# Performance work log

Hardware: AMD Instinct MI355X
Metric: run time of the kernel (lower is better)

The kernel has to match this reference:

```python
import jax, jax.numpy as jnp
import numpy as np

DIM = 768
NUM_HEADS = 12
HEAD_DIM = DIM // NUM_HEADS
BASE = 10000.0


def rotate_half(x):
    x1, x2 = jnp.split(x, 2, axis=-1)
    return jnp.concatenate((-x2, x1), axis=-1)


def rope_cos_sin(seq_len, dim, dtype):
    inv_freq = 1.0 / (BASE ** (jnp.arange(0, dim, 2, dtype=jnp.float32) / dim))
    t = jnp.arange(seq_len, dtype=jnp.float32)
    freqs = jnp.einsum('i,j->ij', t, inv_freq)  # [N, dim/2]
    emb = jnp.concatenate((freqs, freqs), axis=-1)  # [N, dim]
    return jnp.cos(emb).astype(dtype), jnp.sin(emb).astype(dtype)


def setup_inputs() -> dict:
    key = jax.random.key(0)
    k1, k2, k3, k4 = jax.random.split(key, 4)
    B, N, C = 1, 4096, DIM
    x = jax.random.normal(k1, (B, N, C), dtype=jnp.float32)
    s = 1.0 / np.sqrt(C)
    qkv_w = jax.random.normal(k2, (3 * C, C), dtype=jnp.float32) * s
    proj_w = jax.random.normal(k3, (C, C), dtype=jnp.float32) * s
    proj_b = jax.random.normal(k4, (C,), dtype=jnp.float32) * 0.01
    return {"x": x, "qkv_w": qkv_w, "proj_w": proj_w, "proj_b": proj_b}


def reference(x, qkv_w, proj_w, proj_b):
    B, N, C = x.shape
    H, D = NUM_HEADS, HEAD_DIM
    scale = D ** -0.5
    qkv = jnp.einsum('bnc,oc->bno', x, qkv_w)           # [B, N, 3C]
    qkv = qkv.reshape(B, N, 3, H, D).transpose(2, 0, 3, 1, 4)  # [3, B, H, N, D]
    q, k, v = qkv[0], qkv[1], qkv[2]
    cos, sin = rope_cos_sin(N, D, x.dtype)              # [N, D] each
    cos = cos[None, None]                               # [1,1,N,D]
    sin = sin[None, None]
    q = q * cos + rotate_half(q) * sin
    k = k * cos + rotate_half(k) * sin
    attn = jnp.einsum('bhqd,bhkd->bhqk', q, k) * scale  # [B,H,N,N]
    attn = jax.nn.softmax(attn, axis=-1)
    out = jnp.einsum('bhqk,bhkd->bhqd', attn, v)        # [B,H,N,D]
    out = out.transpose(0, 2, 1, 3).reshape(B, N, C)
    return jnp.einsum('bnc,oc->bno', out, proj_w) + proj_b
```

## Files before the change

### kernel.cpp

```cpp
#include <hip/hip_runtime.h>
#include <hip/hip_bf16.h>
#include <math.h>

#define DIM 768
#define NHEADS 12
#define HD 64
#define SEQ 4096
#define KSPLIT 4

typedef __bf16 bf16x8 __attribute__((ext_vector_type(8)));
typedef float f32x4 __attribute__((ext_vector_type(4)));

__device__ inline ushort f2bf(float f) {
    __bf16 b = (__bf16)f;
    union { __bf16 b; ushort u; } v; v.b = b;
    return v.u;
}

__device__ inline ushort f2bf_tw(float f) {
    union { float f; uint u; } v; v.f = f;
    uint r = v.u + 0x7FFF + ((v.u >> 16) & 1);
    return (ushort)(r >> 16);
}

__global__ __launch_bounds__(256)
void cvt_bf16(const float* __restrict__ src, ushort* __restrict__ dst, int n4)
{
    const int i = blockIdx.x * 256 + threadIdx.x;
    if (i >= n4) return;
    const float4 v = ((const float4*)src)[i];
    ushort4 w;
    w.x = f2bf(v.x); w.y = f2bf(v.y); w.z = f2bf(v.z); w.w = f2bf(v.w);
    ((ushort4*)dst)[i] = w;
}

__global__ __launch_bounds__(256)
void rope_tab_k(float2* __restrict__ tab)
{
    const int idx = blockIdx.x * 256 + threadIdx.x;
    const int j = idx & 31;
    const int n = idx >> 5;
    const float invf = (float)pow(10000.0, -(double)j / 32.0);
    const float ang  = (float)n * invf;
    double s, c;
    sincos((double)ang, &s, &c);
    tab[idx] = make_float2((float)c, (float)s);
}

__global__ __launch_bounds__(256)
void gemm_qkv(const ushort* __restrict__ A, const ushort* __restrict__ B,
              const float2* __restrict__ tab,
              ushort* __restrict__ Qb, ushort* __restrict__ Kb,
              ushort* __restrict__ Vp)
{
    constexpr int BM = 128, BN = 128, BK = 64, PAD = 8;
    __shared__ ushort Ah[BM][BK + PAD];
    __shared__ ushort Bh[BN][BK + PAD];

    const int t    = threadIdx.x;
    const int lane = t & 63;
    const int wv   = t >> 6;
    const int wm   = (wv >> 1) * 64;
    const int wn   = (wv & 1) * 64;
    const int m0   = blockIdx.y * BM;
    const int n0   = blockIdx.x * BN;

    f32x4 acc[4][4] = {};

    const int srow = t >> 3;
    const int sseg = (t & 7) * 8;

    for (int k0 = 0; k0 < DIM; k0 += BK) {
        #pragma unroll
        for (int i = 0; i < 4; ++i) {
            const int row = srow + i * 32;
            *(float4*)&Ah[row][sseg] =
                *(const float4*)&A[(size_t)(m0 + row) * DIM + k0 + sseg];
            *(float4*)&Bh[row][sseg] =
                *(const float4*)&B[(size_t)(n0 + row) * DIM + k0 + sseg];
        }
        __syncthreads();

        #pragma unroll
        for (int ks = 0; ks < BK; ks += 32) {
            const int koff = ks + ((lane >> 4) << 3);
            const int rs = lane & 15;
            bf16x8 af[4], bf[4];
            #pragma unroll
            for (int i = 0; i < 4; ++i) {
                af[i] = *(const bf16x8*)&Ah[wm + i * 16 + rs][koff];
                bf[i] = *(const bf16x8*)&Bh[wn + i * 16 + rs][koff];
            }
            #pragma unroll
            for (int i = 0; i < 4; ++i)
                #pragma unroll
                for (int j = 0; j < 4; ++j)
                    acc[i][j] = __builtin_amdgcn_mfma_f32_16x16x32_bf16(
                        af[i], bf[j], acc[i][j], 0, 0, 0);
        }
        __syncthreads();
    }

    const int rsel  = lane & 15;
    const int quad  = lane >> 4;
    const int rbase = m0 + wm + (quad << 2);
    const int c0    = n0 + wn;
    const int tt    = c0 / DIM;
    const int h     = (c0 % DIM) >> 6;

    if (tt == 2) {
        const int T = (m0 + wm) >> 6;
        #pragma unroll
        for (int j = 0; j < 4; ++j) {
            const int d = rsel + 16 * j;
            ushort vv[16];
            #pragma unroll
            for (int r = 0; r < 4; ++r)
                #pragma unroll
                for (int i = 0; i < 4; ++i)
                    vv[4 * r + i] = f2bf(acc[i][j][r]);
            ushort* dst = &Vp[((size_t)h * HD + d) * SEQ + T * 64 + 16 * quad];
            *(float4*)&dst[0] = *(const float4*)&vv[0];
            *(float4*)&dst[8] = *(const float4*)&vv[8];
        }
    } else {
        ushort* dstb = (tt == 0 ? Qb : Kb) + (size_t)h * SEQ * HD;
        const float qs = (tt == 0) ? 0.18033688011112042f : 1.0f;
        #pragma unroll
        for (int i = 0; i < 4; ++i)
            #pragma unroll
            for (int r = 0; r < 4; ++r) {
                const int n = rbase + i * 16 + r;
                #pragma unroll
                for (int j = 0; j < 2; ++j) {
                    const float a = acc[i][j][r];
                    const float b = acc[i][j + 2][r];
                    const float2 cs2 = tab[n * 32 + rsel + 16 * j];
                    dstb[(size_t)n * HD + rsel + 16 * j]      = f2bf((a * cs2.x - b * cs2.y) * qs);
                    dstb[(size_t)n * HD + rsel + 16 * j + 32] = f2bf((b * cs2.x + a * cs2.y) * qs);
                }
            }
    }
}

__global__ __launch_bounds__(256, 4)
void flash_mfma(const ushort* __restrict__ Qb, const ushort* __restrict__ Kb,
                const ushort* __restrict__ Vp,
                float* __restrict__ Opart, float* __restrict__ lpart)
{
    __shared__ ushort Ks[64][68];
    __shared__ ushort Vs[64][68];
    __shared__ ushort Pl[4][32][68];

    const int t    = threadIdx.x;
    const int lane = t & 63;
    const int wv   = t >> 6;
    const int rsel = lane & 15;
    const int quad = lane >> 4;

    const int p  = blockIdx.x + 32 * (blockIdx.y + 12 * blockIdx.z);
    const int c  = p & 7;
    const int r  = p >> 3;
    const int gi = r >> 5;
    const int xq = r & 31;
    const int g  = gi * 8 + c;
    const int h    = g % 12;
    const int part = g / 12;

    const int q0   = xq * 128 + wv * 32;
    const int Tbeg = (part * (SEQ / KSPLIT)) >> 6;
    const int Tend = Tbeg + (SEQ / KSPLIT) / 64;

    const int crow = t >> 2;
    const int ccol = (t & 3) * 16;

    bf16x8 aq[2][2];
    #pragma unroll
    for (int mi = 0; mi < 2; ++mi)
        #pragma unroll
        for (int ks = 0; ks < 2; ++ks)
            aq[mi][ks] = *(const bf16x8*)&Qb[((size_t)h * SEQ + q0 + 16 * mi + rsel) * HD
                                             + ks * 32 + quad * 8];

    f32x4 accO[2][4] = {};
    float lsum[2][4] = {};

    for (int T = Tbeg; T < Tend; ++T) {
        __syncthreads();
        {
            const ushort* ksrc = &Kb[((size_t)h * SEQ + T * 64 + crow) * HD + ccol];
            *(float4*)&Ks[crow][ccol]     = *(const float4*)&ksrc[0];
            *(float4*)&Ks[crow][ccol + 8] = *(const float4*)&ksrc[8];
            const ushort* vsrc = &Vp[((size_t)h * HD + crow) * SEQ + T * 64 + ccol];
            *(float4*)&Vs[crow][ccol]     = *(const float4*)&vsrc[0];
            *(float4*)&Vs[crow][ccol + 8] = *(const float4*)&vsrc[8];
        }
        __syncthreads();

        bf16x8 bk[4][2], bv[4][2];
        #pragma unroll
        for (int n = 0; n < 4; ++n)
            #pragma unroll
            for (int ks = 0; ks < 2; ++ks) {
                bk[n][ks] = *(const bf16x8*)&Ks[16 * n + rsel][32 * ks + quad * 8];
                bv[n][ks] = *(const bf16x8*)&Vs[16 * n + rsel][32 * ks + quad * 8];
            }

        #pragma unroll
        for (int mi = 0; mi < 2; ++mi) {
            f32x4 accS[4] = {};
            #pragma unroll
            for (int ks = 0; ks < 2; ++ks)
                #pragma unroll
                for (int n = 0; n < 4; ++n)
                    accS[n] = __builtin_amdgcn_mfma_f32_16x16x32_bf16(
                        aq[mi][ks], bk[n][ks], accS[n], 0, 0, 0);

            #pragma unroll
            for (int r = 0; r < 4; ++r) {
                const float p0 = __builtin_amdgcn_exp2f(accS[0][r]);
                const float p1 = __builtin_amdgcn_exp2f(accS[1][r]);
                const float p2 = __builtin_amdgcn_exp2f(accS[2][r]);
                const float p3 = __builtin_amdgcn_exp2f(accS[3][r]);
                ushort4 pw;
                pw.x = f2bf_tw(p0); pw.y = f2bf_tw(p1);
                pw.z = f2bf_tw(p2); pw.w = f2bf_tw(p3);
                *(ushort4*)&Pl[wv][16 * mi + 4 * quad + r][4 * rsel] = pw;
                lsum[mi][r] += (p0 + p1) + (p2 + p3);
            }
        }

        asm volatile("s_waitcnt lgkmcnt(0)" ::: "memory");

        #pragma unroll
        for (int mi = 0; mi < 2; ++mi) {
            bf16x8 ap[2];
            ap[0] = *(const bf16x8*)&Pl[wv][16 * mi + rsel][quad * 8];
            ap[1] = *(const bf16x8*)&Pl[wv][16 * mi + rsel][32 + quad * 8];
            #pragma unroll
            for (int ks = 0; ks < 2; ++ks)
                #pragma unroll
                for (int j = 0; j < 4; ++j)
                    accO[mi][j] = __builtin_amdgcn_mfma_f32_16x16x32_bf16(
                        ap[ks], bv[j][ks], accO[mi][j], 0, 0, 0);
        }
    }

    #pragma unroll
    for (int mi = 0; mi < 2; ++mi)
        #pragma unroll
        for (int r = 0; r < 4; ++r) {
            float s = lsum[mi][r];
            s += __shfl_xor(s, 1);
            s += __shfl_xor(s, 2);
            s += __shfl_xor(s, 4);
            s += __shfl_xor(s, 8);
            lsum[mi][r] = s;
        }

    float* Ob = Opart + ((size_t)part * NHEADS + h) * SEQ * HD;
    float* lb = lpart + ((size_t)part * NHEADS + h) * SEQ;
    #pragma unroll
    for (int mi = 0; mi < 2; ++mi)
        #pragma unroll
        for (int r = 0; r < 4; ++r) {
            const int n = q0 + 16 * mi + 4 * quad + r;
            #pragma unroll
            for (int j = 0; j < 4; ++j)
                Ob[(size_t)n * HD + 16 * j + rsel] = accO[mi][j][r];
            if (rsel == 0) lb[n] = lsum[mi][r];
        }
}

__global__ __launch_bounds__(256)
void merge_k(const float* __restrict__ Opart, const float* __restrict__ lpart,
             ushort* __restrict__ AO)
{
    const int idx = blockIdx.x * 256 + threadIdx.x;
    const int dg = idx & 15;
    const int n  = (idx >> 4) & (SEQ - 1);
    const int h  = idx >> 16;

    float4 o = make_float4(0.f, 0.f, 0.f, 0.f);
    float l = 0.f;
    #pragma unroll
    for (int p = 0; p < KSPLIT; ++p) {
        const float4 v = *(const float4*)&Opart[(((size_t)p * NHEADS + h) * SEQ + n) * HD + dg * 4];
        o.x += v.x; o.y += v.y; o.z += v.z; o.w += v.w;
        l += lpart[((size_t)p * NHEADS + h) * SEQ + n];
    }
    const float inv = 1.f / l;
    ushort4 w;
    w.x = f2bf(o.x * inv); w.y = f2bf(o.y * inv);
    w.z = f2bf(o.z * inv); w.w = f2bf(o.w * inv);
    *(ushort4*)&AO[(size_t)n * DIM + h * HD + dg * 4] = w;
}

__global__ __launch_bounds__(256)
void gemm_proj(const ushort* __restrict__ A, const ushort* __restrict__ B,
               const float* __restrict__ bias, float* __restrict__ out)
{
    constexpr int BM = 128, BN = 128, BK = 64, PAD = 8;
    __shared__ ushort As[BM][BK + PAD];
    __shared__ ushort Bs[BN][BK + PAD];

    const int t    = threadIdx.x;
    const int lane = t & 63;
    const int wv   = t >> 6;
    const int wm   = (wv >> 1) * 64;
    const int wn   = (wv & 1) * 64;
    const int m0   = blockIdx.y * BM;
    const int n0   = blockIdx.x * BN;

    f32x4 acc[4][4] = {};

    const int srow = t >> 3;
    const int sseg = (t & 7) * 8;

    for (int k0 = 0; k0 < DIM; k0 += BK) {
        #pragma unroll
        for (int i = 0; i < 4; ++i) {
            const int row = srow + i * 32;
            *(float4*)&As[row][sseg] =
                *(const float4*)&A[(size_t)(m0 + row) * DIM + k0 + sseg];
            *(float4*)&Bs[row][sseg] =
                *(const float4*)&B[(size_t)(n0 + row) * DIM + k0 + sseg];
        }
        __syncthreads();

        #pragma unroll
        for (int ks = 0; ks < BK; ks += 32) {
            const int koff = ks + ((lane >> 4) << 3);
            const int rs = lane & 15;
            bf16x8 af[4], bf[4];
            #pragma unroll
            for (int i = 0; i < 4; ++i) {
                af[i] = *(const bf16x8*)&As[wm + i * 16 + rs][koff];
                bf[i] = *(const bf16x8*)&Bs[wn + i * 16 + rs][koff];
            }
            #pragma unroll
            for (int i = 0; i < 4; ++i)
                #pragma unroll
                for (int j = 0; j < 4; ++j)
                    acc[i][j] = __builtin_amdgcn_mfma_f32_16x16x32_bf16(
                        af[i], bf[j], acc[i][j], 0, 0, 0);
        }
        __syncthreads();
    }

    const int rbase = m0 + wm + ((lane >> 4) << 2);
    const int cbase = n0 + wn + (lane & 15);

    #pragma unroll
    for (int j = 0; j < 4; ++j) {
        const int col = cbase + j * 16;
        const float bv = bias[col];
        #pragma unroll
        for (int i = 0; i < 4; ++i) {
            const int row0 = rbase + i * 16;
            #pragma unroll
            for (int r = 0; r < 4; ++r)
                out[(size_t)(row0 + r) * DIM + col] = acc[i][j][r] + bv;
        }
    }
}

extern "C" void kernel_launch(void* const* d_in, const int* in_sizes, int n_in,
                              void* d_out, int out_size, void* d_ws, size_t ws_size,
                              hipStream_t stream)
{
    const float* x      = (const float*)d_in[0];
    const float* qkv_w  = (const float*)d_in[1];
    const float* proj_w = (const float*)d_in[2];
    const float* proj_b = (const float*)d_in[3];

    const size_t headsz = (size_t)NHEADS * SEQ * HD;
    char* p = (char*)d_ws;
    ushort* Qb    = (ushort*)p;                 p += headsz * 2;
    ushort* Kb    = (ushort*)p;                 p += headsz * 2;
    ushort* Vp    = (ushort*)p;                 p += headsz * 2;
    ushort* AO    = (ushort*)p;                 p += (size_t)SEQ * DIM * 2;
    float*  Opart = (float*)p;                  p += (size_t)KSPLIT * headsz * 4;
    float*  lpart = (float*)p;                  p += (size_t)KSPLIT * NHEADS * SEQ * 4;
    float2* tab   = (float2*)p;                 p += (size_t)SEQ * 32 * sizeof(float2);
    ushort* xb    = (ushort*)p;                 p += (size_t)SEQ * DIM * 2;
    ushort* qwb   = (ushort*)p;                 p += (size_t)3 * DIM * DIM * 2;
    ushort* pwb   = (ushort*)p;
    float*  out   = (float*)d_out;

    rope_tab_k<<<(SEQ * 32) / 256, 256, 0, stream>>>(tab);
    cvt_bf16<<<(SEQ * DIM / 4) / 256, 256, 0, stream>>>(x, xb, SEQ * DIM / 4);
    cvt_bf16<<<(3 * DIM * DIM / 4) / 256, 256, 0, stream>>>(qkv_w, qwb, 3 * DIM * DIM / 4);
    cvt_bf16<<<(DIM * DIM / 4) / 256, 256, 0, stream>>>(proj_w, pwb, DIM * DIM / 4);

    gemm_qkv<<<dim3(3 * DIM / 128, SEQ / 128), 256, 0, stream>>>(
        xb, qwb, tab, Qb, Kb, Vp);

    flash_mfma<<<dim3(SEQ / 128, NHEADS, KSPLIT), 256, 0, stream>>>(
        Qb, Kb, Vp, Opart, lpart);

    merge_k<<<(NHEADS * SEQ * 16) / 256, 256, 0, stream>>>(Opart, lpart, AO);

    gemm_proj<<<dim3(DIM / 128, SEQ / 128), 256, 0, stream>>>(
        AO, pwb, proj_b, out);
}
```

Baseline: 223.0 us.

## Double-buffer K/V tiles in flash attention with register prefetch

Adds a second LDS buffer for the K and V tiles. The next tile's global loads are issued into registers at the top of each iteration and written to the alternate buffer after the compute, leaving one barrier per iteration instead of two. The goal is to hide global load latency behind the MFMA and softmax work. In exchange it uses more LDS and registers, and the launch-bounds occupancy hint drops from 4 to 3 blocks per CU.

```diff
diff --git a/kernel.cpp b/kernel.cpp
--- a/kernel.cpp
+++ b/kernel.cpp
@@ -143,13 +143,13 @@
     }
 }
 
-__global__ __launch_bounds__(256, 4)
+__global__ __launch_bounds__(256, 3)
 void flash_mfma(const ushort* __restrict__ Qb, const ushort* __restrict__ Kb,
                 const ushort* __restrict__ Vp,
                 float* __restrict__ Opart, float* __restrict__ lpart)
 {
-    __shared__ ushort Ks[64][68];
-    __shared__ ushort Vs[64][68];
+    __shared__ ushort Ks[2][64][68];
+    __shared__ ushort Vs[2][64][68];
     __shared__ ushort Pl[4][32][68];
 
     const int t    = threadIdx.x;
@@ -185,25 +185,37 @@
     f32x4 accO[2][4] = {};
     float lsum[2][4] = {};
 
+    {
+        const ushort* ksrc = &Kb[((size_t)h * SEQ + Tbeg * 64 + crow) * HD + ccol];
+        const float4 k0 = *(const float4*)&ksrc[0];
+        const float4 k1 = *(const float4*)&ksrc[8];
+        const ushort* vsrc = &Vp[((size_t)h * HD + crow) * SEQ + Tbeg * 64 + ccol];
+        const float4 v0 = *(const float4*)&vsrc[0];
+        const float4 v1 = *(const float4*)&vsrc[8];
+        *(float4*)&Ks[0][crow][ccol]     = k0;
+        *(float4*)&Ks[0][crow][ccol + 8] = k1;
+        *(float4*)&Vs[0][crow][ccol]     = v0;
+        *(float4*)&Vs[0][crow][ccol + 8] = v1;
+    }
+    __syncthreads();
+
+    int cur = 0;
     for (int T = Tbeg; T < Tend; ++T) {
-        __syncthreads();
-        {
-            const ushort* ksrc = &Kb[((size_t)h * SEQ + T * 64 + crow) * HD + ccol];
-            *(float4*)&Ks[crow][ccol]     = *(const float4*)&ksrc[0];
-            *(float4*)&Ks[crow][ccol + 8] = *(const float4*)&ksrc[8];
-            const ushort* vsrc = &Vp[((size_t)h * HD + crow) * SEQ + T * 64 + ccol];
-            *(float4*)&Vs[crow][ccol]     = *(const float4*)&vsrc[0];
-            *(float4*)&Vs[crow][ccol + 8] = *(const float4*)&vsrc[8];
-        }
-        __syncthreads();
+        const int Tn = (T + 1 < Tend) ? T + 1 : T;
+        const ushort* ksrc = &Kb[((size_t)h * SEQ + Tn * 64 + crow) * HD + ccol];
+        const float4 kn0 = *(const float4*)&ksrc[0];
+        const float4 kn1 = *(const float4*)&ksrc[8];
+        const ushort* vsrc = &Vp[((size_t)h * HD + crow) * SEQ + Tn * 64 + ccol];
+        const float4 vn0 = *(const float4*)&vsrc[0];
+        const float4 vn1 = *(const float4*)&vsrc[8];
 
         bf16x8 bk[4][2], bv[4][2];
         #pragma unroll
         for (int n = 0; n < 4; ++n)
             #pragma unroll
             for (int ks = 0; ks < 2; ++ks) {
-                bk[n][ks] = *(const bf16x8*)&Ks[16 * n + rsel][32 * ks + quad * 8];
-                bv[n][ks] = *(const bf16x8*)&Vs[16 * n + rsel][32 * ks + quad * 8];
+                bk[n][ks] = *(const bf16x8*)&Ks[cur][16 * n + rsel][32 * ks + quad * 8];
+                bv[n][ks] = *(const bf16x8*)&Vs[cur][16 * n + rsel][32 * ks + quad * 8];
             }
 
         #pragma unroll
@@ -244,6 +256,13 @@
                     accO[mi][j] = __builtin_amdgcn_mfma_f32_16x16x32_bf16(
                         ap[ks], bv[j][ks], accO[mi][j], 0, 0, 0);
         }
+
+        *(float4*)&Ks[cur ^ 1][crow][ccol]     = kn0;
+        *(float4*)&Ks[cur ^ 1][crow][ccol + 8] = kn1;
+        *(float4*)&Vs[cur ^ 1][crow][ccol]     = vn0;
+        *(float4*)&Vs[cur ^ 1][crow][ccol + 8] = vn1;
+        __syncthreads();
+        cur ^= 1;
     }
 
     #pragma unroll
```

New measurement: 213.2 us. 4.4% less time.
